# Performance work log

Hardware: AMD Instinct MI355X
Metric: run time of the kernel (lower is better)

## Reference

```python
import jax, jax.numpy as jnp
import numpy as np

B, S, D, H = 2, 2048, 1024, 16
DK = D // H
THETA = 10000.0


def apply_rope(t, pos):
    # t: [B, H, S, DK], pos: [B, S] int
    half = DK // 2
    inv_freq = THETA ** (-jnp.arange(0, DK, 2, dtype=jnp.float32) / DK)  # [half]
    ang = pos.astype(jnp.float32)[:, None, :, None] * inv_freq  # [B,1,S,half]
    cos, sin = jnp.cos(ang), jnp.sin(ang)
    t1, t2 = t[..., 0::2], t[..., 1::2]  # interleaved pairs
    r1 = t1 * cos - t2 * sin
    r2 = t1 * sin + t2 * cos
    return jnp.stack([r1, r2], axis=-1).reshape(t.shape)


def setup_inputs() -> dict:
    key = jax.random.key(0)
    ks = jax.random.split(key, 5)
    x = jax.random.normal(ks[0], (B, S, D), dtype=jnp.float32)
    scale = 0.02
    Wq = jax.random.normal(ks[1], (D, D), dtype=jnp.float32) * scale
    Wk = jax.random.normal(ks[2], (D, D), dtype=jnp.float32) * scale
    Wv = jax.random.normal(ks[3], (D, D), dtype=jnp.float32) * scale
    Wo = jax.random.normal(ks[4], (D, D), dtype=jnp.float32) * scale
    token_positions = jnp.broadcast_to(jnp.arange(S, dtype=jnp.int64), (B, S))
    return {"x": x, "Wq": Wq, "Wk": Wk, "Wv": Wv, "Wo": Wo,
            "token_positions": token_positions}


def reference(x, Wq, Wk, Wv, Wo, token_positions):
    # Bias-free linear projections: y = x @ W^T (torch Linear convention)
    q = jnp.einsum('bsd,ed->bse', x, Wq)
    k = jnp.einsum('bsd,ed->bse', x, Wk)
    v = jnp.einsum('bsd,ed->bse', x, Wv)
    # split heads: [B, S, H*DK] -> [B, H, S, DK]
    def split(t):
        return t.reshape(B, S, H, DK).transpose(0, 2, 1, 3)
    qh, kh, vh = split(q), split(k), split(v)
    qh = apply_rope(qh, token_positions)
    kh = apply_rope(kh, token_positions)
    scores = jnp.einsum('bhqd,bhkd->bhqk', qh, kh) / jnp.sqrt(jnp.float32(DK))
    causal = jnp.tril(jnp.ones((S, S), dtype=bool))
    scores = jnp.where(causal, scores, jnp.finfo(scores.dtype).min)
    probs = jax.nn.softmax(scores, axis=-1)
    out = jnp.einsum('bhqk,bhkd->bhqd', probs, vh)  # [B,H,S,DK]
    out = out.transpose(0, 2, 1, 3).reshape(B, S, D)
    return jnp.einsum('bsd,ed->bse', out, Wo)
```

## Files before the change

### kernel.cpp

```cpp
#include <hip/hip_runtime.h>
#include <stdint.h>

#define B_  2
#define S_  2048
#define D_  1024
#define H_  16
#define DK_ 64

using bf16x8 = __attribute__((ext_vector_type(8))) short;
using f32x4  = __attribute__((ext_vector_type(4))) float;

__device__ __forceinline__ unsigned short f2bf(float f) {
    union { float f; uint32_t u; } v; v.f = f;
    uint32_t r = v.u + 0x7FFFu + ((v.u >> 16) & 1u);
    return (unsigned short)(r >> 16);
}

__device__ __forceinline__ uint32_t cvtpk(float lo, float hi) {
    uint32_t r;
    asm("v_cvt_pk_bf16_f32 %0, %1, %2" : "=v"(r) : "v"(lo), "v"(hi));
    return r;
}
__device__ __forceinline__ void ps32(uint32_t& a, uint32_t& b) {
    asm volatile("v_permlane32_swap_b32 %0, %1" : "+v"(a), "+v"(b));
}
__device__ __forceinline__ void ps16(uint32_t& a, uint32_t& b) {
    asm volatile("v_permlane16_swap_b32 %0, %1" : "+v"(a), "+v"(b));
}

#define GLD16(G, L) __builtin_amdgcn_global_load_lds( \
    (const __attribute__((address_space(1))) void*)(const void*)(G), \
    (__attribute__((address_space(3))) void*)(void*)(L), 16, 0, 0)

__global__ __launch_bounds__(256) void k_prep(
    const float* __restrict__ x,
    const float* __restrict__ Wq, const float* __restrict__ Wk,
    const float* __restrict__ Wv, const float* __restrict__ Wo,
    unsigned short* __restrict__ xb,
    unsigned short* __restrict__ wqb, unsigned short* __restrict__ wkb,
    unsigned short* __restrict__ wvb, unsigned short* __restrict__ wob)
{
    const int bid = blockIdx.x, tid = threadIdx.x;
    const float* s;
    unsigned short* d;
    int i;
    if (bid < 4096) {
        s = x; d = xb; i = bid * 256 + tid;
    } else {
        const int w = (bid - 4096) >> 10;
        s = w == 0 ? Wq : w == 1 ? Wk : w == 2 ? Wv : Wo;
        d = w == 0 ? wqb : w == 1 ? wkb : w == 2 ? wvb : wob;
        i = ((bid - 4096) & 1023) * 256 + tid;
    }
    float4 v = ((const float4*)s)[i];
    union { unsigned short u[4]; uint2 dd; } o;
    o.u[0] = f2bf(v.x); o.u[1] = f2bf(v.y); o.u[2] = f2bf(v.z); o.u[3] = f2bf(v.w);
    ((uint2*)d)[i] = o.dd;
}

template<int MODE, int TM>
__global__ __launch_bounds__(256) void k_gemm_bt(
    const unsigned short* __restrict__ A,
    const unsigned short* __restrict__ W0,
    const unsigned short* __restrict__ W1,
    const unsigned short* __restrict__ W2,
    void* __restrict__ C0, void* __restrict__ C1, void* __restrict__ C2,
    int M, int N, int K)
{
    constexpr int MI  = TM / 32;
    constexpr int ACH = TM / 64;
    __shared__ __align__(16) unsigned short As[2][TM * 32];
    __shared__ __align__(16) unsigned short Bs[2][128 * 32];

    const int tid  = threadIdx.x;
    const int wid  = tid >> 6, lane = tid & 63;
    const int m16  = lane & 15, g = lane >> 4;
    const int m0   = blockIdx.x * TM, n0 = blockIdx.y * 128;
    const unsigned short* Wm = blockIdx.z == 0 ? W0 : (blockIdx.z == 1 ? W1 : W2);
    void* Cm = blockIdx.z == 0 ? C0 : (blockIdx.z == 1 ? C1 : C2);

    const int wm = (wid >> 1) * (TM / 2), wn = (wid & 1) * 64;
    const int srow = lane >> 2;
    const int scol = ((lane & 3) ^ ((lane >> 3) & 3)) * 8;
    const int sw8  = (m16 >> 1) & 3;

    const f32x4 fz = {0.f, 0.f, 0.f, 0.f};
    f32x4 acc[MI][4];
#pragma unroll
    for (int i = 0; i < MI; ++i)
#pragma unroll
        for (int j = 0; j < 4; ++j) acc[i][j] = fz;

#pragma unroll
    for (int c = 0; c < ACH; ++c) {
        const int chunk = wid * ACH + c;
        GLD16(A + (size_t)(m0 + chunk * 16 + srow) * K + scol, &As[0][chunk * 512]);
    }
#pragma unroll
    for (int c = 0; c < 2; ++c) {
        const int chunk = wid * 2 + c;
        GLD16(Wm + (size_t)(n0 + chunk * 16 + srow) * K + scol, &Bs[0][chunk * 512]);
    }
    __syncthreads();

    int buf = 0;
    for (int k0 = 0; k0 < K; k0 += 32) {
        if (k0 + 32 < K) {
#pragma unroll
            for (int c = 0; c < ACH; ++c) {
                const int chunk = wid * ACH + c;
                GLD16(A + (size_t)(m0 + chunk * 16 + srow) * K + k0 + 32 + scol,
                      &As[buf ^ 1][chunk * 512]);
            }
#pragma unroll
            for (int c = 0; c < 2; ++c) {
                const int chunk = wid * 2 + c;
                GLD16(Wm + (size_t)(n0 + chunk * 16 + srow) * K + k0 + 32 + scol,
                      &Bs[buf ^ 1][chunk * 512]);
            }
        }
        bf16x8 af[MI], bf[4];
#pragma unroll
        for (int i = 0; i < MI; ++i)
            af[i] = *(const bf16x8*)(&As[buf][(wm + i * 16 + m16) * 32 + ((g ^ sw8) * 8)]);
#pragma unroll
        for (int j = 0; j < 4; ++j)
            bf[j] = *(const bf16x8*)(&Bs[buf][(wn + j * 16 + m16) * 32 + ((g ^ sw8) * 8)]);
#pragma unroll
        for (int i = 0; i < MI; ++i)
#pragma unroll
            for (int j = 0; j < 4; ++j)
                acc[i][j] = __builtin_amdgcn_mfma_f32_16x16x32_bf16(af[i], bf[j], acc[i][j], 0, 0, 0);
        __syncthreads();
        buf ^= 1;
    }

#pragma unroll
    for (int i = 0; i < MI; ++i) {
#pragma unroll
        for (int j = 0; j < 4; ++j) {
            if (MODE == 1) {
#pragma unroll
                for (int r = 0; r < 4; ++r) {
                    const int row = m0 + wm + i * 16 + g * 4 + r;
                    const int col = n0 + wn + j * 16 + m16;
                    ((float*)Cm)[(size_t)row * N + col] = acc[i][j][r];
                }
            } else if (blockIdx.z == 2) {
                const int row0 = m0 + wm + i * 16 + g * 4;
                const int col  = n0 + wn + j * 16 + m16;
                const int b = row0 >> 11, s0 = row0 & (S_ - 1);
                const int h = col >> 6,  dk = col & (DK_ - 1);
                union { unsigned short u[4]; uint2 d; } p4;
#pragma unroll
                for (int r = 0; r < 4; ++r) p4.u[r] = f2bf(acc[i][j][r]);
                *(uint2*)((unsigned short*)Cm
                          + ((size_t)((b * H_ + h) * DK_ + dk)) * S_ + s0) = p4.d;
            } else {
#pragma unroll
                for (int r = 0; r < 4; ++r) {
                    const int row = m0 + wm + i * 16 + g * 4 + r;
                    const int col = n0 + wn + j * 16 + m16;
                    const int b = row >> 11, s = row & (S_ - 1);
                    const int h = col >> 6,  dk = col & (DK_ - 1);
                    ((unsigned short*)Cm)[((size_t)((b * H_ + h) * S_ + s)) * DK_ + dk]
                        = f2bf(acc[i][j][r]);
                }
            }
        }
    }
}

__global__ __launch_bounds__(256) void k_rope_inplace(
    unsigned short* __restrict__ qh, unsigned short* __restrict__ kh,
    const int* __restrict__ tok)
{
    const int idx = blockIdx.x * 256 + threadIdx.x;
    const int c = idx & 7;
    const int s = (idx >> 3) & (S_ - 1);
    const int b = idx >> 18;
    const size_t off = (size_t)idx * 8;
    const float SC = 0.18033688011112042f;

    const float pos = (float)tok[b * S_ + s];
    float cs[4], sn[4];
#pragma unroll
    for (int i = 0; i < 4; ++i) {
        const int p = c * 4 + i;
        const float inv = exp2f((float)(-2 * p) * (13.287712379549449f / 64.f));
        sincosf(pos * inv, &sn[i], &cs[i]);
    }
    bf16x8 qv = *(bf16x8*)(qh + off);
    bf16x8 kv = *(bf16x8*)(kh + off);
    bf16x8 qo, ko;
#pragma unroll
    for (int i = 0; i < 4; ++i) {
        union { uint32_t u; float f; } q1{(uint32_t)(unsigned short)qv[2*i] << 16};
        union { uint32_t u; float f; } q2{(uint32_t)(unsigned short)qv[2*i+1] << 16};
        qo[2 * i]     = (short)f2bf((q1.f * cs[i] - q2.f * sn[i]) * SC);
        qo[2 * i + 1] = (short)f2bf((q1.f * sn[i] + q2.f * cs[i]) * SC);
        union { uint32_t u; float f; } k1{(uint32_t)(unsigned short)kv[2*i] << 16};
        union { uint32_t u; float f; } k2{(uint32_t)(unsigned short)kv[2*i+1] << 16};
        ko[2 * i]     = (short)f2bf(k1.f * cs[i] - k2.f * sn[i]);
        ko[2 * i + 1] = (short)f2bf(k1.f * sn[i] + k2.f * cs[i]);
    }
    *(bf16x8*)(qh + off) = qo;
    *(bf16x8*)(kh + off) = ko;
}

__global__ __launch_bounds__(256, 2) void k_fattn6c(
    const unsigned short* __restrict__ Q,
    const unsigned short* __restrict__ K,
    const unsigned short* __restrict__ Vt,
    unsigned short* __restrict__ O)
{
    __shared__ __align__(16) unsigned short Ks[2][64 * 64];
    __shared__ __align__(16) unsigned short Vs[2][64 * 64];

    const int tid = threadIdx.x, wid = tid >> 6, lane = tid & 63;
    const int m16 = lane & 15, g = lane >> 4;
    const int bh = blockIdx.x & 31;
    const int j  = blockIdx.x >> 5;
    const int b = bh >> 4, h = bh & 15;
    const unsigned short* Qb = Q  + (size_t)bh * S_ * DK_;
    const unsigned short* Kb = K  + (size_t)bh * S_ * DK_;
    const unsigned short* Vb = Vt + (size_t)bh * DK_ * S_;

    const int r8   = lane >> 3;
    const int slot = (lane & 7) ^ r8;
    const int ch0  = wid * 2, ch1 = wid * 2 + 1;

    const f32x4 fz = {0.f, 0.f, 0.f, 0.f};
    union { uint32_t u[4]; bf16x8 v; } one_;
    one_.u[0] = one_.u[1] = one_.u[2] = one_.u[3] = 0x3F803F80u;
    const bf16x8 ones = one_.v;

    GLD16(Kb + (size_t)(ch0 * 8 + r8) * DK_ + slot * 8, &Ks[0][ch0 * 512]);
    GLD16(Kb + (size_t)(ch1 * 8 + r8) * DK_ + slot * 8, &Ks[0][ch1 * 512]);
    GLD16(Vb + (size_t)(ch0 * 8 + r8) * S_  + slot * 8, &Vs[0][ch0 * 512]);
    GLD16(Vb + (size_t)(ch1 * 8 + r8) * S_  + slot * 8, &Vs[0][ch1 * 512]);
    __syncthreads();

    int buf = 0;
#pragma unroll
    for (int ph = 0; ph < 2; ++ph) {
        const int qi = ph ? 31 - j : j;
        const int q0 = qi * 64;
        const int qw0 = q0 + wid * 16;

        bf16x8 qf[2];
        {
            const unsigned short* qp = Qb + (size_t)(qw0 + m16) * DK_ + g * 8;
            qf[0] = *(const bf16x8*)(qp);
            qf[1] = *(const bf16x8*)(qp + 32);
        }

        f32x4 o[4];
#pragma unroll
        for (int i = 0; i < 4; ++i) o[i] = fz;
        f32x4 psacc = fz;

        const int nt = qi + 1;
        for (int t = 0; t < nt; ++t) {
            const int kv0 = t * 64;
            int nkv0 = -1;
            if (t + 1 < nt)      nkv0 = kv0 + 64;
            else if (ph == 0)    nkv0 = 0;
            if (nkv0 >= 0) {
                GLD16(Kb + (size_t)(nkv0 + ch0 * 8 + r8) * DK_ + slot * 8, &Ks[buf ^ 1][ch0 * 512]);
                GLD16(Kb + (size_t)(nkv0 + ch1 * 8 + r8) * DK_ + slot * 8, &Ks[buf ^ 1][ch1 * 512]);
                GLD16(Vb + (size_t)(ch0 * 8 + r8) * S_ + nkv0 + slot * 8, &Vs[buf ^ 1][ch0 * 512]);
                GLD16(Vb + (size_t)(ch1 * 8 + r8) * S_ + nkv0 + slot * 8, &Vs[buf ^ 1][ch1 * 512]);
            }

            f32x4 sc[4];
            __builtin_amdgcn_s_setprio(1);
#pragma unroll
            for (int c = 0; c < 4; ++c) {
                const int row = c * 16 + m16, rr = row & 7;
                bf16x8 kf0 = *(const bf16x8*)(&Ks[buf][row * 64 + ((g ^ rr) << 3)]);
                bf16x8 kf1 = *(const bf16x8*)(&Ks[buf][row * 64 + (((4 + g) ^ rr) << 3)]);
                f32x4 z = fz;
                z = __builtin_amdgcn_mfma_f32_16x16x32_bf16(kf0, qf[0], z, 0, 0, 0);
                z = __builtin_amdgcn_mfma_f32_16x16x32_bf16(kf1, qf[1], z, 0, 0, 0);
                sc[c] = z;
            }
            __builtin_amdgcn_s_setprio(0);

            bf16x8 vf[2][4];
#pragma unroll
            for (int c2 = 0; c2 < 4; ++c2) {
                const int rv = (c2 * 16 + m16) & 7;
                vf[0][c2] = *(const bf16x8*)(&Vs[buf][(c2 * 16 + m16) * 64 + ((g ^ rv) << 3)]);
                vf[1][c2] = *(const bf16x8*)(&Vs[buf][(c2 * 16 + m16) * 64 + (((4 + g) ^ rv) << 3)]);
            }

            const bool maskT = (t == qi);
            const int qrow = qw0 + m16;
            uint32_t pk[4][2];
#pragma unroll
            for (int c = 0; c < 4; ++c) {
                float p[4];
#pragma unroll
                for (int r = 0; r < 4; ++r) {
                    float v = exp2f(sc[c][r]);
                    if (maskT && (kv0 + c * 16 + g * 4 + r > qrow)) v = 0.f;
                    p[r] = v;
                }
                pk[c][0] = cvtpk(p[0], p[1]);
                pk[c][1] = cvtpk(p[2], p[3]);
            }

            bf16x8 pf[2];
#pragma unroll
            for (int ks = 0; ks < 2; ++ks) {
                uint32_t ylo = pk[2 * ks][0], zlo = pk[2 * ks + 1][0];
                ps32(ylo, zlo); ps16(ylo, zlo);
                uint32_t yhi = pk[2 * ks][1], zhi = pk[2 * ks + 1][1];
                ps32(yhi, zhi); ps16(yhi, zhi);
                union { uint32_t u[4]; bf16x8 v; } fu;
                fu.u[0] = ylo; fu.u[1] = yhi; fu.u[2] = zlo; fu.u[3] = zhi;
                pf[ks] = fu.v;
            }

            __builtin_amdgcn_s_setprio(1);
#pragma unroll
            for (int c2 = 0; c2 < 4; ++c2) {
                o[c2] = __builtin_amdgcn_mfma_f32_16x16x32_bf16(pf[0], vf[0][c2], o[c2], 0, 0, 0);
                o[c2] = __builtin_amdgcn_mfma_f32_16x16x32_bf16(pf[1], vf[1][c2], o[c2], 0, 0, 0);
            }
            psacc = __builtin_amdgcn_mfma_f32_16x16x32_bf16(pf[0], ones, psacc, 0, 0, 0);
            psacc = __builtin_amdgcn_mfma_f32_16x16x32_bf16(pf[1], ones, psacc, 0, 0, 0);
            __builtin_amdgcn_s_setprio(0);

            __syncthreads();
            buf ^= 1;
        }

        float lrq[4];
#pragma unroll
        for (int r = 0; r < 4; ++r)
            lrq[r] = 1.f / psacc[r];
#pragma unroll
        for (int c2 = 0; c2 < 4; ++c2)
#pragma unroll
            for (int r = 0; r < 4; ++r) {
                const int orow = qw0 + g * 4 + r;
                const int ocol = h * DK_ + c2 * 16 + m16;
                O[((size_t)(b * S_ + orow)) * D_ + ocol] = f2bf(o[c2][r] * lrq[r]);
            }
    }
}

extern "C" void kernel_launch(void* const* d_in, const int* in_sizes, int n_in,
                              void* d_out, int out_size, void* d_ws, size_t ws_size,
                              hipStream_t stream) {
    (void)in_sizes; (void)n_in; (void)out_size; (void)ws_size;
    const float* x   = (const float*)d_in[0];
    const float* Wq  = (const float*)d_in[1];
    const float* Wk  = (const float*)d_in[2];
    const float* Wv  = (const float*)d_in[3];
    const float* Wo  = (const float*)d_in[4];
    const int*   tok = (const int*)d_in[5];

    char* ws = (char*)d_ws;
    const size_t MB = 1u << 20;
    unsigned short* xb  = (unsigned short*)(ws + 0 * MB);
    unsigned short* wqb = (unsigned short*)(ws + 8 * MB);
    unsigned short* wkb = (unsigned short*)(ws + 10 * MB);
    unsigned short* wvb = (unsigned short*)(ws + 12 * MB);
    unsigned short* wob = (unsigned short*)(ws + 14 * MB);
    unsigned short* qh  = (unsigned short*)(ws + 16 * MB);
    unsigned short* kh  = (unsigned short*)(ws + 24 * MB);
    unsigned short* vh  = (unsigned short*)(ws + 32 * MB);
    unsigned short* ao  = (unsigned short*)(ws + 40 * MB);

    k_prep<<<8192, 256, 0, stream>>>(x, Wq, Wk, Wv, Wo,
                                     xb, wqb, wkb, wvb, wob);

    k_gemm_bt<0, 128><<<dim3(32, 8, 3), 256, 0, stream>>>(
        xb, wqb, wkb, wvb, qh, kh, vh, B_ * S_, D_, D_);

    k_rope_inplace<<<2048, 256, 0, stream>>>(qh, kh, tok);

    k_fattn6c<<<dim3(512), 256, 0, stream>>>(qh, kh, vh, ao);

    k_gemm_bt<1, 64><<<dim3(64, 8, 1), 256, 0, stream>>>(
        ao, wob, wob, wob, d_out, d_out, d_out, B_ * S_, D_, D_);
}
```

Before: 110.2 us.

## Process paired causal query tiles in one shared KV sweep

The flash-attention kernel now handles both paired query tiles (j and 31-j) in a single pass over K/V. Each K/V tile is loaded into LDS once and used for both tiles, where before the block swept the short tile and then reloaded from zero for the long one. The block-index mapping is also remapped so neighbouring blocks share a head and blocks of differing lengths interleave. The cost is twice the accumulator and Q register state, which raises register pressure under launch_bounds(256,2), plus branch divergence around the short tile's work.

```diff
diff --git a/kernel.cpp b/kernel.cpp
--- a/kernel.cpp
+++ b/kernel.cpp
@@ -208,7 +208,7 @@
     *(bf16x8*)(kh + off) = ko;
 }
 
-__global__ __launch_bounds__(256, 2) void k_fattn6c(
+__global__ __launch_bounds__(256, 2) void k_fattn10(
     const unsigned short* __restrict__ Q,
     const unsigned short* __restrict__ K,
     const unsigned short* __restrict__ Vt,
@@ -219,8 +219,10 @@
 
     const int tid = threadIdx.x, wid = tid >> 6, lane = tid & 63;
     const int m16 = lane & 15, g = lane >> 4;
-    const int bh = blockIdx.x & 31;
-    const int j  = blockIdx.x >> 5;
+    const int id = blockIdx.x;
+    const int aa = id & 7;
+    const int j  = (id >> 8) ? 15 - aa : aa;
+    const int bh = (id >> 3) & 31;
     const int b = bh >> 4, h = bh & 15;
     const unsigned short* Qb = Q  + (size_t)bh * S_ * DK_;
     const unsigned short* Kb = K  + (size_t)bh * S_ * DK_;
@@ -234,6 +236,25 @@
     union { uint32_t u[4]; bf16x8 v; } one_;
     one_.u[0] = one_.u[1] = one_.u[2] = one_.u[3] = 0x3F803F80u;
     const bf16x8 ones = one_.v;
+
+    const int qw0A = j * 64 + wid * 16;
+    const int qw0B = (31 - j) * 64 + wid * 16;
+    bf16x8 qfA[2], qfB[2];
+    {
+        const unsigned short* qp = Qb + (size_t)(qw0A + m16) * DK_ + g * 8;
+        qfA[0] = *(const bf16x8*)(qp);
+        qfA[1] = *(const bf16x8*)(qp + 32);
+    }
+    {
+        const unsigned short* qp = Qb + (size_t)(qw0B + m16) * DK_ + g * 8;
+        qfB[0] = *(const bf16x8*)(qp);
+        qfB[1] = *(const bf16x8*)(qp + 32);
+    }
+
+    f32x4 oA[4], oB[4];
+#pragma unroll
+    for (int i = 0; i < 4; ++i) { oA[i] = fz; oB[i] = fz; }
+    f32x4 psA = fz, psB = fz;
 
     GLD16(Kb + (size_t)(ch0 * 8 + r8) * DK_ + slot * 8, &Ks[0][ch0 * 512]);
     GLD16(Kb + (size_t)(ch1 * 8 + r8) * DK_ + slot * 8, &Ks[0][ch1 * 512]);
@@ -241,76 +262,64 @@
     GLD16(Vb + (size_t)(ch1 * 8 + r8) * S_  + slot * 8, &Vs[0][ch1 * 512]);
     __syncthreads();
 
+    const int nt = 32 - j;
     int buf = 0;
-#pragma unroll
-    for (int ph = 0; ph < 2; ++ph) {
-        const int qi = ph ? 31 - j : j;
-        const int q0 = qi * 64;
-        const int qw0 = q0 + wid * 16;
-
-        bf16x8 qf[2];
+    for (int t = 0; t < nt; ++t) {
+        const int kv0 = t * 64;
+        if (t + 1 < nt) {
+            const int nkv0 = kv0 + 64;
+            GLD16(Kb + (size_t)(nkv0 + ch0 * 8 + r8) * DK_ + slot * 8, &Ks[buf ^ 1][ch0 * 512]);
+            GLD16(Kb + (size_t)(nkv0 + ch1 * 8 + r8) * DK_ + slot * 8, &Ks[buf ^ 1][ch1 * 512]);
+            GLD16(Vb + (size_t)(ch0 * 8 + r8) * S_ + nkv0 + slot * 8, &Vs[buf ^ 1][ch0 * 512]);
+            GLD16(Vb + (size_t)(ch1 * 8 + r8) * S_ + nkv0 + slot * 8, &Vs[buf ^ 1][ch1 * 512]);
+        }
+
+        const bool actA = (t <= j);
+
+        f32x4 scB[4], scA[4];
+        __builtin_amdgcn_s_setprio(1);
+#pragma unroll
+        for (int c = 0; c < 4; ++c) {
+            const int row = c * 16 + m16, rr = row & 7;
+            bf16x8 kf0 = *(const bf16x8*)(&Ks[buf][row * 64 + ((g ^ rr) << 3)]);
+            bf16x8 kf1 = *(const bf16x8*)(&Ks[buf][row * 64 + (((4 + g) ^ rr) << 3)]);
+            f32x4 z = fz;
+            z = __builtin_amdgcn_mfma_f32_16x16x32_bf16(kf0, qfB[0], z, 0, 0, 0);
+            z = __builtin_amdgcn_mfma_f32_16x16x32_bf16(kf1, qfB[1], z, 0, 0, 0);
+            scB[c] = z;
+            if (actA) {
+                f32x4 za = fz;
+                za = __builtin_amdgcn_mfma_f32_16x16x32_bf16(kf0, qfA[0], za, 0, 0, 0);
+                za = __builtin_amdgcn_mfma_f32_16x16x32_bf16(kf1, qfA[1], za, 0, 0, 0);
+                scA[c] = za;
+            }
+        }
+        __builtin_amdgcn_s_setprio(0);
+
+        bf16x8 vf[2][4];
+#pragma unroll
+        for (int c2 = 0; c2 < 4; ++c2) {
+            const int rv = (c2 * 16 + m16) & 7;
+            vf[0][c2] = *(const bf16x8*)(&Vs[buf][(c2 * 16 + m16) * 64 + ((g ^ rv) << 3)]);
+            vf[1][c2] = *(const bf16x8*)(&Vs[buf][(c2 * 16 + m16) * 64 + (((4 + g) ^ rv) << 3)]);
+        }
+
         {
-            const unsigned short* qp = Qb + (size_t)(qw0 + m16) * DK_ + g * 8;
-            qf[0] = *(const bf16x8*)(qp);
-            qf[1] = *(const bf16x8*)(qp + 32);
-        }
-
-        f32x4 o[4];
-#pragma unroll
-        for (int i = 0; i < 4; ++i) o[i] = fz;
-        f32x4 psacc = fz;
-
-        const int nt = qi + 1;
-        for (int t = 0; t < nt; ++t) {
-            const int kv0 = t * 64;
-            int nkv0 = -1;
-            if (t + 1 < nt)      nkv0 = kv0 + 64;
-            else if (ph == 0)    nkv0 = 0;
-            if (nkv0 >= 0) {
-                GLD16(Kb + (size_t)(nkv0 + ch0 * 8 + r8) * DK_ + slot * 8, &Ks[buf ^ 1][ch0 * 512]);
-                GLD16(Kb + (size_t)(nkv0 + ch1 * 8 + r8) * DK_ + slot * 8, &Ks[buf ^ 1][ch1 * 512]);
-                GLD16(Vb + (size_t)(ch0 * 8 + r8) * S_ + nkv0 + slot * 8, &Vs[buf ^ 1][ch0 * 512]);
-                GLD16(Vb + (size_t)(ch1 * 8 + r8) * S_ + nkv0 + slot * 8, &Vs[buf ^ 1][ch1 * 512]);
-            }
-
-            f32x4 sc[4];
-            __builtin_amdgcn_s_setprio(1);
-#pragma unroll
-            for (int c = 0; c < 4; ++c) {
-                const int row = c * 16 + m16, rr = row & 7;
-                bf16x8 kf0 = *(const bf16x8*)(&Ks[buf][row * 64 + ((g ^ rr) << 3)]);
-                bf16x8 kf1 = *(const bf16x8*)(&Ks[buf][row * 64 + (((4 + g) ^ rr) << 3)]);
-                f32x4 z = fz;
-                z = __builtin_amdgcn_mfma_f32_16x16x32_bf16(kf0, qf[0], z, 0, 0, 0);
-                z = __builtin_amdgcn_mfma_f32_16x16x32_bf16(kf1, qf[1], z, 0, 0, 0);
-                sc[c] = z;
-            }
-            __builtin_amdgcn_s_setprio(0);
-
-            bf16x8 vf[2][4];
-#pragma unroll
-            for (int c2 = 0; c2 < 4; ++c2) {
-                const int rv = (c2 * 16 + m16) & 7;
-                vf[0][c2] = *(const bf16x8*)(&Vs[buf][(c2 * 16 + m16) * 64 + ((g ^ rv) << 3)]);
-                vf[1][c2] = *(const bf16x8*)(&Vs[buf][(c2 * 16 + m16) * 64 + (((4 + g) ^ rv) << 3)]);
-            }
-
-            const bool maskT = (t == qi);
-            const int qrow = qw0 + m16;
+            const bool maskT = (t == nt - 1);
+            const int qrow = qw0B + m16;
             uint32_t pk[4][2];
 #pragma unroll
             for (int c = 0; c < 4; ++c) {
                 float p[4];
 #pragma unroll
                 for (int r = 0; r < 4; ++r) {
-                    float v = exp2f(sc[c][r]);
+                    float v = exp2f(scB[c][r]);
                     if (maskT && (kv0 + c * 16 + g * 4 + r > qrow)) v = 0.f;
                     p[r] = v;
                 }
                 pk[c][0] = cvtpk(p[0], p[1]);
                 pk[c][1] = cvtpk(p[2], p[3]);
             }
-
             bf16x8 pf[2];
 #pragma unroll
             for (int ks = 0; ks < 2; ++ks) {
@@ -322,32 +331,83 @@
                 fu.u[0] = ylo; fu.u[1] = yhi; fu.u[2] = zlo; fu.u[3] = zhi;
                 pf[ks] = fu.v;
             }
-
             __builtin_amdgcn_s_setprio(1);
 #pragma unroll
             for (int c2 = 0; c2 < 4; ++c2) {
-                o[c2] = __builtin_amdgcn_mfma_f32_16x16x32_bf16(pf[0], vf[0][c2], o[c2], 0, 0, 0);
-                o[c2] = __builtin_amdgcn_mfma_f32_16x16x32_bf16(pf[1], vf[1][c2], o[c2], 0, 0, 0);
-            }
-            psacc = __builtin_amdgcn_mfma_f32_16x16x32_bf16(pf[0], ones, psacc, 0, 0, 0);
-            psacc = __builtin_amdgcn_mfma_f32_16x16x32_bf16(pf[1], ones, psacc, 0, 0, 0);
+                oB[c2] = __builtin_amdgcn_mfma_f32_16x16x32_bf16(pf[0], vf[0][c2], oB[c2], 0, 0, 0);
+                oB[c2] = __builtin_amdgcn_mfma_f32_16x16x32_bf16(pf[1], vf[1][c2], oB[c2], 0, 0, 0);
+            }
+            psB = __builtin_amdgcn_mfma_f32_16x16x32_bf16(pf[0], ones, psB, 0, 0, 0);
+            psB = __builtin_amdgcn_mfma_f32_16x16x32_bf16(pf[1], ones, psB, 0, 0, 0);
             __builtin_amdgcn_s_setprio(0);
-
-            __syncthreads();
-            buf ^= 1;
-        }
-
+        }
+
+        if (actA) {
+            const bool maskT = (t == j);
+            const int qrow = qw0A + m16;
+            uint32_t pk[4][2];
+#pragma unroll
+            for (int c = 0; c < 4; ++c) {
+                float p[4];
+#pragma unroll
+                for (int r = 0; r < 4; ++r) {
+                    float v = exp2f(scA[c][r]);
+                    if (maskT && (kv0 + c * 16 + g * 4 + r > qrow)) v = 0.f;
+                    p[r] = v;
+                }
+                pk[c][0] = cvtpk(p[0], p[1]);
+                pk[c][1] = cvtpk(p[2], p[3]);
+            }
+            bf16x8 pf[2];
+#pragma unroll
+            for (int ks = 0; ks < 2; ++ks) {
+                uint32_t ylo = pk[2 * ks][0], zlo = pk[2 * ks + 1][0];
+                ps32(ylo, zlo); ps16(ylo, zlo);
+                uint32_t yhi = pk[2 * ks][1], zhi = pk[2 * ks + 1][1];
+                ps32(yhi, zhi); ps16(yhi, zhi);
+                union { uint32_t u[4]; bf16x8 v; } fu;
+                fu.u[0] = ylo; fu.u[1] = yhi; fu.u[2] = zlo; fu.u[3] = zhi;
+                pf[ks] = fu.v;
+            }
+            __builtin_amdgcn_s_setprio(1);
+#pragma unroll
+            for (int c2 = 0; c2 < 4; ++c2) {
+                oA[c2] = __builtin_amdgcn_mfma_f32_16x16x32_bf16(pf[0], vf[0][c2], oA[c2], 0, 0, 0);
+                oA[c2] = __builtin_amdgcn_mfma_f32_16x16x32_bf16(pf[1], vf[1][c2], oA[c2], 0, 0, 0);
+            }
+            psA = __builtin_amdgcn_mfma_f32_16x16x32_bf16(pf[0], ones, psA, 0, 0, 0);
+            psA = __builtin_amdgcn_mfma_f32_16x16x32_bf16(pf[1], ones, psA, 0, 0, 0);
+            __builtin_amdgcn_s_setprio(0);
+        }
+
+        __syncthreads();
+        buf ^= 1;
+    }
+
+    {
         float lrq[4];
 #pragma unroll
-        for (int r = 0; r < 4; ++r)
-            lrq[r] = 1.f / psacc[r];
+        for (int r = 0; r < 4; ++r) lrq[r] = 1.f / psA[r];
 #pragma unroll
         for (int c2 = 0; c2 < 4; ++c2)
 #pragma unroll
             for (int r = 0; r < 4; ++r) {
-                const int orow = qw0 + g * 4 + r;
+                const int orow = qw0A + g * 4 + r;
                 const int ocol = h * DK_ + c2 * 16 + m16;
-                O[((size_t)(b * S_ + orow)) * D_ + ocol] = f2bf(o[c2][r] * lrq[r]);
+                O[((size_t)(b * S_ + orow)) * D_ + ocol] = f2bf(oA[c2][r] * lrq[r]);
+            }
+    }
+    {
+        float lrq[4];
+#pragma unroll
+        for (int r = 0; r < 4; ++r) lrq[r] = 1.f / psB[r];
+#pragma unroll
+        for (int c2 = 0; c2 < 4; ++c2)
+#pragma unroll
+            for (int r = 0; r < 4; ++r) {
+                const int orow = qw0B + g * 4 + r;
+                const int ocol = h * DK_ + c2 * 16 + m16;
+                O[((size_t)(b * S_ + orow)) * D_ + ocol] = f2bf(oB[c2][r] * lrq[r]);
             }
     }
 }
@@ -383,7 +443,7 @@
 
     k_rope_inplace<<<2048, 256, 0, stream>>>(qh, kh, tok);
 
-    k_fattn6c<<<dim3(512), 256, 0, stream>>>(qh, kh, vh, ao);
+    k_fattn10<<<dim3(512), 256, 0, stream>>>(qh, kh, vh, ao);
 
     k_gemm_bt<1, 64><<<dim3(64, 8, 1), 256, 0, stream>>>(
         ao, wob, wob, wob, d_out, d_out, d_out, B_ * S_, D_, D_);
```

Result: slower. 118.4 us (+7.4%).
